# Kernel optimization log

Measured on AMD Instinct MI355X. Metric: run time of the kernel, lower is better.

## Reference

```python
import jax, jax.numpy as jnp
import numpy as np

N_NODES = 50000
N_EDGES = 800000
IN_DIM = 128
OUT_DIM = 128
NEG_INIT = -1e9  # matches torch fill_(-1e9) init for scatter amax
LEAKY_SLOPE = 0.01  # nn.LeakyReLU default


def setup_inputs() -> dict:
    key = jax.random.key(0)
    ks = jax.random.split(key, 8)
    x = jax.random.normal(ks[0], (N_NODES, IN_DIM), dtype=jnp.float32)
    edge_index = jax.random.randint(ks[1], (2, N_EDGES), 0, N_NODES, dtype=jnp.int64)
    edge_weight = jax.random.uniform(ks[2], (N_EDGES,), dtype=jnp.float32)
    # MLP params (nn.Linear default init: U(-1/sqrt(fan_in), 1/sqrt(fan_in)))
    s1 = 1.0 / np.sqrt(IN_DIM)
    s2 = 1.0 / np.sqrt(OUT_DIM)
    w1 = jax.random.uniform(ks[3], (OUT_DIM, IN_DIM), minval=-s1, maxval=s1, dtype=jnp.float32)
    b1 = jax.random.uniform(ks[4], (OUT_DIM,), minval=-s1, maxval=s1, dtype=jnp.float32)
    w2 = jax.random.uniform(ks[5], (OUT_DIM, OUT_DIM), minval=-s2, maxval=s2, dtype=jnp.float32)
    b2 = jax.random.uniform(ks[6], (OUT_DIM,), minval=-s2, maxval=s2, dtype=jnp.float32)
    eps = jnp.zeros((1,), dtype=jnp.float32)
    return {"x": x, "edge_index": edge_index, "edge_weight": edge_weight,
            "w1": w1, "b1": b1, "w2": w2, "b2": b2, "eps": eps}


def reference(x, edge_index, edge_weight, w1, b1, w2, b2, eps):
    src = edge_index[0]
    dst = edge_index[1]
    # gather + optional edge-weight scale: [E, D]
    messages = x[src] * edge_weight[:, None]
    # scatter-max to dst; init at -1e9 so include_self=False semantics hold
    agg = jnp.full(x.shape, NEG_INIT, dtype=x.dtype).at[dst].max(messages)
    agg = jnp.where(agg == NEG_INIT, jnp.zeros_like(agg), agg)  # isolated nodes -> 0
    h = (1.0 + eps) * x + agg  # eps broadcasts ([1])
    h = h @ w1.T + b1
    h = jnp.where(h >= 0, h, LEAKY_SLOPE * h)  # LeakyReLU
    out = h @ w2.T + b2
    return out
```

## Files before the change

### kernel.cpp

```cpp
#include <hip/hip_runtime.h>
#include <stdint.h>

#define NN 50000
#define NE 800000
#define D  128
#define NEG_INIT -1e9f
#define CAP 64
#define OVF_CAP 131072

#define CNT_OFF     64
#define CNT_STRIDE  16
#define OVF_CNT_OFF (CNT_OFF + NN * CNT_STRIDE)
#define OVF_OFF     (OVF_CNT_OFF + 4)
#define BKT_OFF     1062400
#define XBF_OFF     (BKT_OFF + NN * CAP)
#define WBF_OFF     (XBF_OFF + NN * (D / 2))

#define HSTRIDE 136

#define FILL_BLKS 3125
#define PX_BLKS   6250
#define PW_BLKS   32

typedef __attribute__((ext_vector_type(8))) short short8;
typedef __attribute__((ext_vector_type(4))) float float4v;

__device__ __forceinline__ float b2f(uint16_t u) {
    union { uint32_t u; float f; } v; v.u = ((uint32_t)u) << 16; return v.f;
}
__device__ __forceinline__ float ubits(uint32_t u) {
    union { uint32_t u; float f; } v; v.u = u; return v.f;
}
__device__ __forceinline__ uint16_t f2b(float f) {
    union { float f; uint32_t u; } v; v.f = f;
    uint32_t r = v.u + 0x7fffu + ((v.u >> 16) & 1u);
    return (uint16_t)(r >> 16);
}

__device__ __forceinline__ void block_probe(const uint16_t* __restrict__ xraw,
                                            const int* __restrict__ eraw,
                                            int* sflags) {
    int t = threadIdx.x;
    if (t < 64) {
        float v0 = b2f(xraw[2 * t]);
        float v1 = b2f(xraw[2 * t + 1]);
        int bad = (!(v0 > -1e4f && v0 < 1e4f)) || (!(v1 > -1e4f && v1 < 1e4f));
        unsigned long long bm = __ballot(bad);
        int nz = (t < 32) ? (eraw[2 * t + 1] != 0) : 0;
        unsigned long long im = __ballot(nz);
        if (t == 0) { sflags[0] = bm ? 1 : 0; sflags[1] = im ? 0 : 1; }
    }
    __syncthreads();
}

__global__ __launch_bounds__(256) void prep_fill_kernel(
    const uint16_t* __restrict__ xraw,
    const int*      __restrict__ eraw,
    const uint16_t* __restrict__ ewraw,
    const uint16_t* __restrict__ w1raw,
    const uint16_t* __restrict__ w2raw,
    int* __restrict__ ws)
{
    __shared__ int sflags[2];
    block_probe(xraw, eraw, sflags);
    const int f32 = sflags[0], i64 = sflags[1];

    int bid = blockIdx.x;
    if (bid < FILL_BLKS) {
        int e = bid * 256 + threadIdx.x;
        int src, dst;
        if (i64) {
            const long long* e64 = (const long long*)eraw;
            src = (int)e64[e];
            dst = (int)e64[NE + e];
        } else {
            src = eraw[e];
            dst = eraw[NE + e];
        }
        if ((unsigned)src >= NN || (unsigned)dst >= NN) return;
        uint w = f32 ? (uint)f2b(((const float*)ewraw)[e]) : (uint)ewraw[e];
        uint entry = (w << 16) | (uint)src;
        int slot = atomicAdd(ws + CNT_OFF + dst * CNT_STRIDE, 1);
        if (slot < CAP) {
            ((uint*)(ws + BKT_OFF))[(size_t)dst * CAP + slot] = entry;
        } else {
            int o = atomicAdd(ws + OVF_CNT_OFF, 1);
            if (o < OVF_CAP) {
                ws[OVF_OFF + 2 * o]     = dst;
                ws[OVF_OFF + 2 * o + 1] = (int)entry;
            }
        }
    } else if (bid < FILL_BLKS + PX_BLKS) {
        int i4 = ((bid - FILL_BLKS) * 256 + threadIdx.x) * 4;
        ushort* dst = (ushort*)(ws + XBF_OFF);
        if (f32) {
            float4 v = *(const float4*)((const float*)xraw + i4);
            ushort4 o; o.x = f2b(v.x); o.y = f2b(v.y); o.z = f2b(v.z); o.w = f2b(v.w);
            *(ushort4*)(dst + i4) = o;
        } else {
            *(ushort4*)(dst + i4) = *(const ushort4*)(xraw + i4);
        }
    } else {
        int i4 = ((bid - FILL_BLKS - PX_BLKS) * 256 + threadIdx.x) * 4;
        const uint16_t* src = (i4 < 16384) ? w1raw : w2raw;
        int off = i4 & 16383;
        ushort* dst = (ushort*)(ws + WBF_OFF);
        if (f32) {
            float4 v = *(const float4*)((const float*)src + off);
            ushort4 o; o.x = f2b(v.x); o.y = f2b(v.y); o.z = f2b(v.z); o.w = f2b(v.w);
            *(ushort4*)(dst + i4) = o;
        } else {
            *(ushort4*)(dst + i4) = *(const ushort4*)(src + off);
        }
    }
}

__global__ __launch_bounds__(256) void gmlp_kernel(
    const uint16_t* __restrict__ xraw,
    const int*      __restrict__ eraw,
    const uint16_t* __restrict__ b1raw,
    const uint16_t* __restrict__ b2raw,
    const uint16_t* __restrict__ epsraw,
    const int* __restrict__ ws,
    uint16_t* __restrict__ outraw)
{
    __shared__ int    sflags[2];
    __shared__ uint   tl[16 * (HSTRIDE / 2)];
    __shared__ ushort hl[16 * HSTRIDE];

    block_probe(xraw, eraw, sflags);
    const int f32 = sflags[0];

    const int tid  = threadIdx.x;
    const int wave = tid >> 6;
    const int lane = tid & 63;
    const int m    = lane & 15;
    const int quad = lane >> 4;
    const int node0 = blockIdx.x * 16;

    const ushort* w1b = (const ushort*)(ws + WBF_OFF);
    const ushort* w2b = w1b + 16384;
    const uint*   xbf = (const uint*)(ws + XBF_OFF);
    const uint*   bkt = (const uint*)(ws + BKT_OFF);

    const float eps1 = 1.0f + (f32 ? ((const float*)epsraw)[0] : b2f(epsraw[0]));

    int cr[4];
    #pragma unroll
    for (int j = 0; j < 4; ++j)
        cr[j] = ws[CNT_OFF + (wave * 4 + j + node0) * CNT_STRIDE];

    for (int j = 0; j < 4; ++j) {
        int nl = wave * 4 + j;
        int n  = node0 + nl;
        int cnt_raw = cr[j];
        int cnt = (cnt_raw < CAP) ? cnt_raw : CAP;

        float m0[16], m1[16];
        #pragma unroll
        for (int u = 0; u < 16; ++u) { m0[u] = NEG_INIT; m1[u] = NEG_INIT; }

        const uint* brow = bkt + (size_t)n * CAP;
        for (int i = 0; i < cnt; i += 16) {
            uint4 q[4];
            #pragma unroll
            for (int qq = 0; qq < 4; ++qq) q[qq] = *(const uint4*)(brow + i + qq * 4);
            #pragma unroll
            for (int u = 0; u < 16; ++u) {
                uint e0  = ((const uint*)q)[u];
                uint idx = e0 & 0xffffu;
                idx = min(idx, (uint)(NN - 1));
                uint v = xbf[idx * 64 + lane];
                float w  = ubits(e0 & 0xffff0000u);
                float p0 = ubits(v << 16) * w;
                float p1 = ubits(v & 0xffff0000u) * w;
                m0[u] = fmaxf(m0[u], p0);
                m1[u] = fmaxf(m1[u], p1);
            }
        }
        if (cnt_raw > CAP) {
            int novf = ws[OVF_CNT_OFF];
            if (novf > OVF_CAP) novf = OVF_CAP;
            for (int o = 0; o < novf; ++o) {
                if (ws[OVF_OFF + 2 * o] == n) {
                    uint e0 = (uint)ws[OVF_OFF + 2 * o + 1];
                    uint v  = xbf[(e0 & 0xffff) * 64 + lane];
                    float w = b2f((uint16_t)(e0 >> 16));
                    m0[0] = fmaxf(m0[0], b2f((uint16_t)v) * w);
                    m1[0] = fmaxf(m1[0], b2f((uint16_t)(v >> 16)) * w);
                }
            }
        }
        #pragma unroll
        for (int u = 8; u > 0; u >>= 1)
            #pragma unroll
            for (int v2 = 0; v2 < u; ++v2) {
                m0[v2] = fmaxf(m0[v2], m0[v2 + u]);
                m1[v2] = fmaxf(m1[v2], m1[v2 + u]);
            }
        float mx = m0[0], my = m1[0];
        if (cnt_raw == 0) { mx = 0.f; my = 0.f; }

        uint xv = xbf[(size_t)n * 64 + lane];
        float t0 = eps1 * b2f((uint16_t)xv) + mx;
        float t1 = eps1 * b2f((uint16_t)(xv >> 16)) + my;
        tl[nl * (HSTRIDE / 2) + lane] = (uint)f2b(t0) | ((uint)f2b(t1) << 16);
    }
    __syncthreads();

    short8 a[4];
    {
        const ushort* arow = (const ushort*)tl + m * HSTRIDE + quad * 8;
        #pragma unroll
        for (int kb = 0; kb < 4; ++kb) a[kb] = *(const short8*)(arow + kb * 32);
    }

    #pragma unroll
    for (int t = 0; t < 2; ++t) {
        int ct = wave * 2 + t;
        float4v c = {0.f, 0.f, 0.f, 0.f};
        const ushort* brow = w1b + (size_t)(ct * 16 + m) * 128 + quad * 8;
        #pragma unroll
        for (int kb = 0; kb < 4; ++kb)
            c = __builtin_amdgcn_mfma_f32_16x16x32_bf16(a[kb], *(const short8*)(brow + kb * 32), c, 0, 0, 0);
        float bias = f32 ? ((const float*)b1raw)[ct * 16 + m] : b2f(b1raw[ct * 16 + m]);
        #pragma unroll
        for (int r = 0; r < 4; ++r) {
            float v = c[r] + bias;
            v = (v >= 0.f) ? v : 0.01f * v;
            hl[(quad * 4 + r) * HSTRIDE + ct * 16 + m] = f2b(v);
        }
    }
    __syncthreads();

    short8 ah[4];
    {
        const ushort* hrow = hl + m * HSTRIDE + quad * 8;
        #pragma unroll
        for (int kb = 0; kb < 4; ++kb) ah[kb] = *(const short8*)(hrow + kb * 32);
    }

    #pragma unroll
    for (int t = 0; t < 2; ++t) {
        int ct = wave * 2 + t;
        float4v c = {0.f, 0.f, 0.f, 0.f};
        const ushort* brow = w2b + (size_t)(ct * 16 + m) * 128 + quad * 8;
        #pragma unroll
        for (int kb = 0; kb < 4; ++kb)
            c = __builtin_amdgcn_mfma_f32_16x16x32_bf16(ah[kb], *(const short8*)(brow + kb * 32), c, 0, 0, 0);
        float bias = f32 ? ((const float*)b2raw)[ct * 16 + m] : b2f(b2raw[ct * 16 + m]);
        #pragma unroll
        for (int r = 0; r < 4; ++r) {
            float v = c[r] + bias;
            size_t o = (size_t)(node0 + quad * 4 + r) * 128 + ct * 16 + m;
            if (f32) ((float*)outraw)[o] = v;
            else     outraw[o] = f2b(v);
        }
    }
}

extern "C" void kernel_launch(void* const* d_in, const int* in_sizes, int n_in,
                              void* d_out, int out_size, void* d_ws, size_t ws_size,
                              hipStream_t stream) {
    const uint16_t* x    = (const uint16_t*)d_in[0];
    const int*      eidx = (const int*)     d_in[1];
    const uint16_t* ew   = (const uint16_t*)d_in[2];
    const uint16_t* w1   = (const uint16_t*)d_in[3];
    const uint16_t* b1   = (const uint16_t*)d_in[4];
    const uint16_t* w2   = (const uint16_t*)d_in[5];
    const uint16_t* b2   = (const uint16_t*)d_in[6];
    const uint16_t* eps  = (const uint16_t*)d_in[7];
    uint16_t*       out  = (uint16_t*)d_out;
    int* ws = (int*)d_ws;

    hipMemsetAsync((char*)d_ws + (size_t)CNT_OFF * 4, 0,
                   ((size_t)NN * CNT_STRIDE + 1) * 4, stream);
    hipMemsetAsync((char*)d_ws + (size_t)BKT_OFF * 4, 0xFF,
                   (size_t)NN * CAP * 4, stream);
    prep_fill_kernel<<<FILL_BLKS + PX_BLKS + PW_BLKS, 256, 0, stream>>>(
        x, eidx, ew, w1, w2, ws);
    gmlp_kernel<<<NN / 16, 256, 0, stream>>>(x, eidx, b1, b2, eps, ws, out);
}
```

Measured before the change: 203.4 us.

## Switch gather-max path and MLP to fp16 with packed f16 math

Measured after the change: 195.5 us. 1.04x faster.

```diff
diff --git a/kernel.cpp b/kernel.cpp
--- a/kernel.cpp
+++ b/kernel.cpp
@@ -4,17 +4,15 @@
 #define NN 50000
 #define NE 800000
 #define D  128
-#define NEG_INIT -1e9f
 #define CAP 64
 #define OVF_CAP 131072
 
 #define CNT_OFF     64
-#define CNT_STRIDE  16
-#define OVF_CNT_OFF (CNT_OFF + NN * CNT_STRIDE)
+#define OVF_CNT_OFF (CNT_OFF + NN)
 #define OVF_OFF     (OVF_CNT_OFF + 4)
-#define BKT_OFF     1062400
-#define XBF_OFF     (BKT_OFF + NN * CAP)
-#define WBF_OFF     (XBF_OFF + NN * (D / 2))
+#define BKT_OFF     312320
+#define XH_OFF      (BKT_OFF + NN * CAP)
+#define WH_OFF      (XH_OFF + 65536 * (D / 2))
 
 #define HSTRIDE 136
 
@@ -22,19 +20,22 @@
 #define PX_BLKS   6250
 #define PW_BLKS   32
 
-typedef __attribute__((ext_vector_type(8))) short short8;
+typedef _Float16 half8 __attribute__((ext_vector_type(8)));
 typedef __attribute__((ext_vector_type(4))) float float4v;
 
 __device__ __forceinline__ float b2f(uint16_t u) {
     union { uint32_t u; float f; } v; v.u = ((uint32_t)u) << 16; return v.f;
-}
-__device__ __forceinline__ float ubits(uint32_t u) {
-    union { uint32_t u; float f; } v; v.u = u; return v.f;
 }
 __device__ __forceinline__ uint16_t f2b(float f) {
     union { float f; uint32_t u; } v; v.f = f;
     uint32_t r = v.u + 0x7fffu + ((v.u >> 16) & 1u);
     return (uint16_t)(r >> 16);
+}
+__device__ __forceinline__ ushort f2h(float f) {
+    union { _Float16 h; ushort u; } v; v.h = (_Float16)f; return v.u;
+}
+__device__ __forceinline__ float h2f(ushort u) {
+    union { ushort u; _Float16 h; } v; v.u = u; return (float)v.h;
 }
 
 __device__ __forceinline__ void block_probe(const uint16_t* __restrict__ xraw,
@@ -78,13 +79,13 @@
             dst = eraw[NE + e];
         }
         if ((unsigned)src >= NN || (unsigned)dst >= NN) return;
-        uint w = f32 ? (uint)f2b(((const float*)ewraw)[e]) : (uint)ewraw[e];
+        uint w = f32 ? (uint)f2h(((const float*)ewraw)[e]) : (uint)f2h(b2f(ewraw[e]));
         uint entry = (w << 16) | (uint)src;
-        int slot = atomicAdd(ws + CNT_OFF + dst * CNT_STRIDE, 1);
+        int slot = atomicAdd(ws + CNT_OFF + dst, 1) + 1;
         if (slot < CAP) {
             ((uint*)(ws + BKT_OFF))[(size_t)dst * CAP + slot] = entry;
         } else {
-            int o = atomicAdd(ws + OVF_CNT_OFF, 1);
+            int o = atomicAdd(ws + OVF_CNT_OFF, 1) + 1;
             if (o < OVF_CAP) {
                 ws[OVF_OFF + 2 * o]     = dst;
                 ws[OVF_OFF + 2 * o + 1] = (int)entry;
@@ -92,25 +93,31 @@
         }
     } else if (bid < FILL_BLKS + PX_BLKS) {
         int i4 = ((bid - FILL_BLKS) * 256 + threadIdx.x) * 4;
-        ushort* dst = (ushort*)(ws + XBF_OFF);
+        ushort* dst = (ushort*)(ws + XH_OFF);
         if (f32) {
             float4 v = *(const float4*)((const float*)xraw + i4);
-            ushort4 o; o.x = f2b(v.x); o.y = f2b(v.y); o.z = f2b(v.z); o.w = f2b(v.w);
-            *(ushort4*)(dst + i4) = o;
-        } else {
-            *(ushort4*)(dst + i4) = *(const ushort4*)(xraw + i4);
+            ushort4 o; o.x = f2h(v.x); o.y = f2h(v.y); o.z = f2h(v.z); o.w = f2h(v.w);
+            *(ushort4*)(dst + i4) = o;
+        } else {
+            ushort4 v = *(const ushort4*)(xraw + i4);
+            ushort4 o; o.x = f2h(b2f(v.x)); o.y = f2h(b2f(v.y));
+            o.z = f2h(b2f(v.z)); o.w = f2h(b2f(v.w));
+            *(ushort4*)(dst + i4) = o;
         }
     } else {
         int i4 = ((bid - FILL_BLKS - PX_BLKS) * 256 + threadIdx.x) * 4;
         const uint16_t* src = (i4 < 16384) ? w1raw : w2raw;
         int off = i4 & 16383;
-        ushort* dst = (ushort*)(ws + WBF_OFF);
+        ushort* dst = (ushort*)(ws + WH_OFF);
         if (f32) {
             float4 v = *(const float4*)((const float*)src + off);
-            ushort4 o; o.x = f2b(v.x); o.y = f2b(v.y); o.z = f2b(v.z); o.w = f2b(v.w);
-            *(ushort4*)(dst + i4) = o;
-        } else {
-            *(ushort4*)(dst + i4) = *(const ushort4*)(src + off);
+            ushort4 o; o.x = f2h(v.x); o.y = f2h(v.y); o.z = f2h(v.z); o.w = f2h(v.w);
+            *(ushort4*)(dst + i4) = o;
+        } else {
+            ushort4 v = *(const ushort4*)(src + off);
+            ushort4 o; o.x = f2h(b2f(v.x)); o.y = f2h(b2f(v.y));
+            o.z = f2h(b2f(v.z)); o.w = f2h(b2f(v.w));
+            *(ushort4*)(dst + i4) = o;
         }
     }
 }
@@ -138,27 +145,28 @@
     const int quad = lane >> 4;
     const int node0 = blockIdx.x * 16;
 
-    const ushort* w1b = (const ushort*)(ws + WBF_OFF);
-    const ushort* w2b = w1b + 16384;
-    const uint*   xbf = (const uint*)(ws + XBF_OFF);
+    const ushort* w1h = (const ushort*)(ws + WH_OFF);
+    const ushort* w2h = w1h + 16384;
+    const uint*   xh  = (const uint*)(ws + XH_OFF);
     const uint*   bkt = (const uint*)(ws + BKT_OFF);
+    const uint    lane4 = (uint)lane * 4;
 
     const float eps1 = 1.0f + (f32 ? ((const float*)epsraw)[0] : b2f(epsraw[0]));
 
     int cr[4];
     #pragma unroll
     for (int j = 0; j < 4; ++j)
-        cr[j] = ws[CNT_OFF + (wave * 4 + j + node0) * CNT_STRIDE];
+        cr[j] = ws[CNT_OFF + node0 + wave * 4 + j];
 
     for (int j = 0; j < 4; ++j) {
         int nl = wave * 4 + j;
         int n  = node0 + nl;
-        int cnt_raw = cr[j];
-        int cnt = (cnt_raw < CAP) ? cnt_raw : CAP;
-
-        float m0[16], m1[16];
-        #pragma unroll
-        for (int u = 0; u < 16; ++u) { m0[u] = NEG_INIT; m1[u] = NEG_INIT; }
+        int deg = cr[j] + 1;
+        int cnt = (deg < CAP) ? deg : CAP;
+
+        uint mm[16];
+        #pragma unroll
+        for (int u = 0; u < 16; ++u) mm[u] = 0xFFFFFFFFu;
 
         const uint* brow = bkt + (size_t)n * CAP;
         for (int i = 0; i < cnt; i += 16) {
@@ -168,86 +176,85 @@
             #pragma unroll
             for (int u = 0; u < 16; ++u) {
                 uint e0  = ((const uint*)q)[u];
-                uint idx = e0 & 0xffffu;
-                idx = min(idx, (uint)(NN - 1));
-                uint v = xbf[idx * 64 + lane];
-                float w  = ubits(e0 & 0xffff0000u);
-                float p0 = ubits(v << 16) * w;
-                float p1 = ubits(v & 0xffff0000u) * w;
-                m0[u] = fmaxf(m0[u], p0);
-                m1[u] = fmaxf(m1[u], p1);
+                uint off = ((e0 & 0xffffu) << 8) + lane4;
+                uint v   = *(const uint*)((const char*)xh + off);
+                uint p;
+                asm("v_pk_mul_f16 %0, %1, %2 op_sel:[0,1] op_sel_hi:[1,1]"
+                    : "=v"(p) : "v"(v), "v"(e0));
+                asm("v_pk_max_f16 %0, %0, %1" : "+v"(mm[u]) : "v"(p));
             }
         }
-        if (cnt_raw > CAP) {
-            int novf = ws[OVF_CNT_OFF];
+        #pragma unroll
+        for (int u = 8; u > 0; u >>= 1)
+            #pragma unroll
+            for (int v2 = 0; v2 < u; ++v2)
+                asm("v_pk_max_f16 %0, %0, %1" : "+v"(mm[v2]) : "v"(mm[v2 + u]));
+
+        float mx = h2f((ushort)(mm[0] & 0xffffu));
+        float my = h2f((ushort)(mm[0] >> 16));
+
+        if (deg > CAP) {
+            int novf = ws[OVF_CNT_OFF] + 1;
             if (novf > OVF_CAP) novf = OVF_CAP;
             for (int o = 0; o < novf; ++o) {
                 if (ws[OVF_OFF + 2 * o] == n) {
                     uint e0 = (uint)ws[OVF_OFF + 2 * o + 1];
-                    uint v  = xbf[(e0 & 0xffff) * 64 + lane];
-                    float w = b2f((uint16_t)(e0 >> 16));
-                    m0[0] = fmaxf(m0[0], b2f((uint16_t)v) * w);
-                    m1[0] = fmaxf(m1[0], b2f((uint16_t)(v >> 16)) * w);
+                    uint v  = xh[(e0 & 0xffffu) * 64 + lane];
+                    float w = h2f((ushort)(e0 >> 16));
+                    mx = fmaxf(mx, h2f((ushort)(v & 0xffffu)) * w);
+                    my = fmaxf(my, h2f((ushort)(v >> 16)) * w);
                 }
             }
         }
-        #pragma unroll
-        for (int u = 8; u > 0; u >>= 1)
-            #pragma unroll
-            for (int v2 = 0; v2 < u; ++v2) {
-                m0[v2] = fmaxf(m0[v2], m0[v2 + u]);
-                m1[v2] = fmaxf(m1[v2], m1[v2 + u]);
-            }
-        float mx = m0[0], my = m1[0];
-        if (cnt_raw == 0) { mx = 0.f; my = 0.f; }
-
-        uint xv = xbf[(size_t)n * 64 + lane];
-        float t0 = eps1 * b2f((uint16_t)xv) + mx;
-        float t1 = eps1 * b2f((uint16_t)(xv >> 16)) + my;
-        tl[nl * (HSTRIDE / 2) + lane] = (uint)f2b(t0) | ((uint)f2b(t1) << 16);
+        if (deg == 0) { mx = 0.f; my = 0.f; }
+
+        uint xv = xh[(size_t)n * 64 + lane];
+        float t0 = eps1 * h2f((ushort)(xv & 0xffffu)) + mx;
+        float t1 = eps1 * h2f((ushort)(xv >> 16)) + my;
+        tl[nl * (HSTRIDE / 2) + lane] = (uint)f2h(t0) | ((uint)f2h(t1) << 16);
     }
     __syncthreads();
 
-    short8 a[4];
+    half8 a[4];
     {
         const ushort* arow = (const ushort*)tl + m * HSTRIDE + quad * 8;
         #pragma unroll
-        for (int kb = 0; kb < 4; ++kb) a[kb] = *(const short8*)(arow + kb * 32);
+        for (int kb = 0; kb < 4; ++kb) a[kb] = *(const half8*)(arow + kb * 32);
     }
 
     #pragma unroll
     for (int t = 0; t < 2; ++t) {
         int ct = wave * 2 + t;
         float4v c = {0.f, 0.f, 0.f, 0.f};
-        const ushort* brow = w1b + (size_t)(ct * 16 + m) * 128 + quad * 8;
+        const ushort* brow = w1h + (size_t)(ct * 16 + m) * 128 + quad * 8;
         #pragma unroll
         for (int kb = 0; kb < 4; ++kb)
-            c = __builtin_amdgcn_mfma_f32_16x16x32_bf16(a[kb], *(const short8*)(brow + kb * 32), c, 0, 0, 0);
+            c = __builtin_amdgcn_mfma_f32_16x16x32_f16(a[kb], *(const half8*)(brow + kb * 32), c, 0, 0, 0);
         float bias = f32 ? ((const float*)b1raw)[ct * 16 + m] : b2f(b1raw[ct * 16 + m]);
         #pragma unroll
         for (int r = 0; r < 4; ++r) {
             float v = c[r] + bias;
             v = (v >= 0.f) ? v : 0.01f * v;
-            hl[(quad * 4 + r) * HSTRIDE + ct * 16 + m] = f2b(v);
+            hl[(quad * 4 + r) * HSTRIDE + ct * 16 + m] = f2h(v);
         }
     }
     __syncthreads();
 
-    short8 ah[4];
+    half8 ah[4];
     {
         const ushort* hrow = hl + m * HSTRIDE + quad * 8;
         #pragma unroll
-        for (int kb = 0; kb < 4; ++kb) ah[kb] = *(const short8*)(hrow + kb * 32);
+        for (int kb = 0; kb < 4; ++kb) ah[kb] = *(const half8*)(hrow + kb * 32);
     }
 
     #pragma unroll
     for (int t = 0; t < 2; ++t) {
         int ct = wave * 2 + t;
         float4v c = {0.f, 0.f, 0.f, 0.f};
-        const ushort* brow = w2b + (size_t)(ct * 16 + m) * 128 + quad * 8;
+        const ushort* brow = w2h + (size_t)(ct * 16 + m) * 128 + quad * 8;
         #pragma unroll
         for (int kb = 0; kb < 4; ++kb)
-            c = __builtin_amdgcn_mfma_f32_16x16x32_bf16(ah[kb], *(const short8*)(brow + kb * 32), c, 0, 0, 0);
+            c = __builtin_amdgcn_mfma_f32_16x16x32_f16(ah[kb], *(const half8*)(brow + kb * 32), c, 0, 0, 0);
         float bias = f32 ? ((const float*)b2raw)[ct * 16 + m] : b2f(b2raw[ct * 16 + m]);
         #pragma unroll
         for (int r = 0; r < 4; ++r) {
@@ -273,10 +280,8 @@
     uint16_t*       out  = (uint16_t*)d_out;
     int* ws = (int*)d_ws;
 
-    hipMemsetAsync((char*)d_ws + (size_t)CNT_OFF * 4, 0,
-                   ((size_t)NN * CNT_STRIDE + 1) * 4, stream);
-    hipMemsetAsync((char*)d_ws + (size_t)BKT_OFF * 4, 0xFF,
-                   (size_t)NN * CAP * 4, stream);
+    hipMemsetAsync((char*)d_ws + (size_t)CNT_OFF * 4, 0xFF,
+                   (size_t)(BKT_OFF + (size_t)NN * CAP - CNT_OFF) * 4, stream);
     prep_fill_kernel<<<FILL_BLKS + PX_BLKS + PW_BLKS, 256, 0, stream>>>(
         x, eidx, ew, w1, w2, ws);
     gmlp_kernel<<<NN / 16, 256, 0, stream>>>(x, eidx, b1, b2, eps, ws, out);
```
